# Optimization experiments

Measured on AMD Instinct MI355X. Metric: run time of the kernel, lower is better.

Reference implementation:

```python
import jax, jax.numpy as jnp
import numpy as np

B, IN, H = 16384, 1024, 1024


def setup_inputs() -> dict:
    key = jax.random.key(0)
    ks = jax.random.split(key, 7)
    s_in = 1.0 / np.sqrt(IN)
    s_h = 1.0 / np.sqrt(H)
    return {
        "x": jax.random.normal(ks[0], (B, IN), jnp.float32),
        "h0": jax.random.normal(ks[1], (B, H), jnp.float32),
        "c0": jax.random.normal(ks[2], (B, H), jnp.float32),
        # gate order along leading dim: f, i, o, g
        "wi": jax.random.uniform(ks[3], (4, H, IN), jnp.float32, -s_in, s_in),
        "bi": jax.random.uniform(ks[4], (4, H), jnp.float32, -s_in, s_in),
        "wh": jax.random.uniform(ks[5], (4, H, H), jnp.float32, -s_h, s_h),
        "bh": jax.random.uniform(ks[6], (4, H), jnp.float32, -s_h, s_h),
    }


def reference(x, h0, c0, wi, bi, wh, bh):
    # pre-activations for all 4 gates in two fused GEMMs: [b, 4, h]
    z = (jnp.einsum("bi,ghi->bgh", x, wi) + bi
         + jnp.einsum("bj,ghj->bgh", h0, wh) + bh)
    f = jax.nn.sigmoid(z[:, 0])   # forget gate
    i = jax.nn.sigmoid(z[:, 1])   # input gate
    o = jax.nn.sigmoid(z[:, 2])   # output gate
    g = jnp.tanh(z[:, 3])         # candidates
    ct = f * c0 + i * g
    ht = o * jnp.tanh(ct)
    return ht, ct
```

## Files before the change

### kernel.cpp

```cpp
#include <hip/hip_runtime.h>
#include <hip/hip_bf16.h>
#include <stdint.h>

#define B_ROWS 16384
#define K_DIM  2048
#define H_DIM  1024
#define N_DIM  4096
#define KB     (K_DIM * 2)
#define NT     (K_DIM / 64)
#define BUF0   0u
#define BUF1   65536u

using f32x4  = __attribute__((ext_vector_type(4))) float;
using bf16x8 = __attribute__((ext_vector_type(8))) __bf16;

__device__ __forceinline__ unsigned short f2bf(float f) {
    union { float f; unsigned u; } v; v.f = f;
    unsigned r = v.u + 0x7fffu + ((v.u >> 16) & 1u);
    return (unsigned short)(r >> 16);
}

__device__ __forceinline__ void gload16(const void* g, const void* l) {
    __builtin_amdgcn_global_load_lds(
        (const __attribute__((address_space(1))) void*)g,
        (__attribute__((address_space(3))) void*)l,
        16, 0, 0);
}

__device__ __forceinline__ float rcp1p(float e) {
    return __builtin_amdgcn_rcpf(1.f + e);
}

__global__ void pack_a_kernel(const float* __restrict__ x, const float* __restrict__ h0,
                              unsigned short* __restrict__ A) {
    int tid = blockIdx.x * 256 + threadIdx.x;
    int64_t idx = (int64_t)tid * 4;
    int b = (int)(idx >> 11);
    int k = (int)(idx & 2047);
    const float* src = (k < 1024) ? (x + (int64_t)b * 1024 + k)
                                  : (h0 + (int64_t)b * 1024 + (k - 1024));
    float4 v = *(const float4*)src;
    ushort4 o;
    o.x = f2bf(v.x); o.y = f2bf(v.y); o.z = f2bf(v.z); o.w = f2bf(v.w);
    *(ushort4*)(A + idx) = o;
}

__global__ void pack_w_kernel(const float* __restrict__ wi, const float* __restrict__ wh,
                              const float* __restrict__ bi, const float* __restrict__ bh,
                              unsigned short* __restrict__ W, float* __restrict__ bias) {
    int tid = blockIdx.x * 256 + threadIdx.x;
    int64_t idx = (int64_t)tid * 4;
    int r = (int)(idx >> 11);
    int k = (int)(idx & 2047);
    int h = r >> 2, g = r & 3;
    const float* src = (k < 1024)
        ? (wi + (int64_t)g * 1048576 + (int64_t)h * 1024 + k)
        : (wh + (int64_t)g * 1048576 + (int64_t)h * 1024 + (k - 1024));
    float4 v = *(const float4*)src;
    ushort4 o;
    o.x = f2bf(v.x); o.y = f2bf(v.y); o.z = f2bf(v.z); o.w = f2bf(v.w);
    *(ushort4*)(W + idx) = o;
    if (k == 0) bias[r] = bi[g * 1024 + h] + bh[g * 1024 + h];
}


#define FENCE   asm volatile("" ::: "memory")
#define BARRIER do { FENCE; __builtin_amdgcn_s_barrier(); FENCE; } while (0)
#define VM2     asm volatile("s_waitcnt vmcnt(2)" ::: "memory")
#define LGKM4   asm volatile("s_waitcnt lgkmcnt(4)" ::: "memory")
#define LGKM8   asm volatile("s_waitcnt lgkmcnt(8)" ::: "memory")
#define SP1     __builtin_amdgcn_s_setprio(1)
#define SP0     __builtin_amdgcn_s_setprio(0)

__global__ __launch_bounds__(512, 2) void lstm_gemm_fused(
    const unsigned short* __restrict__ A, const unsigned short* __restrict__ W,
    const float* __restrict__ bias, const float* __restrict__ c0,
    float* __restrict__ ht, float* __restrict__ ct)
{
    __shared__ char sm[131072];

    const int tid = threadIdx.x;
    const int l   = tid & 63;
    const int w   = tid >> 6;
    const int wm  = w >> 2;
    const int wn  = w & 3;

    const int bid = blockIdx.x;
    const int nid = (bid & 7) * 128 + (bid >> 3);
    const int bm  = nid >> 4;
    const int bn  = nid & 15;

    f32x4 acc[8][4];
#pragma unroll
    for (int i = 0; i < 8; ++i)
#pragma unroll
        for (int j = 0; j < 4; ++j) acc[i][j] = (f32x4){0.f, 0.f, 0.f, 0.f};

    const int srow = w * 16 + (l >> 2);
    const int scb  = ((l & 3) << 4) ^ (l & 32);
    const char* Asrc = (const char*)A + (size_t)(bm * 256 + srow) * KB + scb;
    const char* Wsrc = (const char*)W + (size_t)(bn * 256 + srow) * KB + scb;
    const uint32_t wL = (uint32_t)w * 1024u;

#define STAGE_A(KK, BOFF) do { \
    gload16(Asrc + (KK) * 64,            sm + (BOFF) + (KK) * 16384u + wL); \
    gload16(Asrc + (KK) * 64 + 128 * KB, sm + (BOFF) + (KK) * 16384u + 8192u + wL); \
} while (0)
#define STAGE_B(KK, BOFF) do { \
    gload16(Wsrc + (KK) * 64,            sm + (BOFF) + 32768u + (KK) * 16384u + wL); \
    gload16(Wsrc + (KK) * 64 + 128 * KB, sm + (BOFF) + 32768u + (KK) * 16384u + 8192u + wL); \
} while (0)
#define BUMP do { Asrc += 128; Wsrc += 128; } while (0)

    const int rr = l & 15, kg = l >> 4;
    const uint32_t loff = (uint32_t)rr * 64u + (((uint32_t)kg * 16u) ^ (uint32_t)((rr & 8) << 2));
    const uint32_t Ard = (uint32_t)wm * 8192u + loff;
    const uint32_t Brd = 32768u + (uint32_t)wn * 4096u + loff;

    bf16x8 aL0[4], aH0[4], aL1[4], aH1[4], bb0[4], bb1[4];

#define RD_A4(BOFF, KK, MB, ARR) do { \
    _Pragma("unroll") \
    for (int i_ = 0; i_ < 4; ++i_) \
        ARR[i_] = *(const bf16x8*)(sm + (BOFF) + (KK) * 16384u + Ard + ((MB) + i_) * 1024u); \
} while (0)
#define RD_B4(BOFF, KK, BRR) do { \
    _Pragma("unroll") \
    for (int i_ = 0; i_ < 4; ++i_) \
        BRR[i_] = *(const bf16x8*)(sm + (BOFF) + (KK) * 16384u + Brd + i_ * 1024u); \
} while (0)

#define MFMA16H(ARR, MB, BRR) do { \
    _Pragma("unroll") \
    for (int mf_ = 0; mf_ < 4; ++mf_) \
        _Pragma("unroll") \
        for (int nf_ = 0; nf_ < 4; ++nf_) \
            acc[(MB) + mf_][nf_] = __builtin_amdgcn_mfma_f32_16x16x32_bf16( \
                ARR[mf_], BRR[nf_], acc[(MB) + mf_][nf_], 0, 0, 0); \
} while (0)

    STAGE_A(0, BUF0); STAGE_B(0, BUF0);
    STAGE_A(1, BUF0); STAGE_B(1, BUF0);
    BUMP;
    asm volatile("s_waitcnt vmcnt(4)" ::: "memory");
    BARRIER;
    RD_A4(BUF0, 0, 0, aL0); RD_B4(BUF0, 0, bb0);

#define DO_TILE(CUR, NXT) do { \
     \
    RD_A4(CUR, 0, 4, aH0); \
    STAGE_A(0, NXT); \
    VM2; BARRIER; LGKM4; SP1; MFMA16H(aL0, 0, bb0); SP0; \
     \
    RD_A4(CUR, 1, 0, aL1); RD_B4(CUR, 1, bb1); \
    STAGE_B(0, NXT); \
    BARRIER; LGKM8; SP1; MFMA16H(aH0, 4, bb0); SP0; \
     \
    RD_A4(CUR, 1, 4, aH1); \
    STAGE_A(1, NXT); \
    VM2; BARRIER; LGKM4; SP1; MFMA16H(aL1, 0, bb1); SP0; \
     \
    RD_A4(NXT, 0, 0, aL0); RD_B4(NXT, 0, bb0); \
    STAGE_B(1, NXT); \
    BUMP; \
    BARRIER; LGKM8; SP1; MFMA16H(aH1, 4, bb1); SP0; \
} while (0)

#pragma unroll 1
    for (int tt = 0; tt < NT; tt += 2) {
        DO_TILE(BUF0, BUF1);
        DO_TILE(BUF1, BUF0);
    }

    asm volatile("s_waitcnt vmcnt(0) lgkmcnt(0)" ::: "memory");
    BARRIER;

    float* ep = (float*)(void*)sm + w * 1088;
    const int hbase = bn * 64 + wn * 16;
    const int rbase = bm * 256 + wm * 128;

#pragma unroll
    for (int mf = 0; mf < 8; ++mf) {
#pragma unroll
        for (int nf = 0; nf < 4; ++nf)
#pragma unroll
            for (int r = 0; r < 4; ++r)
                ep[((l >> 4) * 4 + r) * 68 + nf * 16 + (l & 15)] = acc[mf][nf][r];

#pragma unroll
        for (int it = 0; it < 4; ++it) {
            const int row = (l >> 4) + it * 4;
            const int hs  = l & 15;
            f32x4 z = *(const f32x4*)(ep + row * 68 + hs * 4);
            const int hg = hbase + hs;
            const float4 bz = ((const float4*)bias)[hg];
            const int brow = rbase + mf * 16 + row;

            float zf = z.x + bz.x;
            float zi = z.y + bz.y;
            float zo = z.z + bz.z;
            float zg = z.w + bz.w;

            float fg = rcp1p(__expf(-zf));
            float ig = rcp1p(__expf(-zi));
            float og = rcp1p(__expf(-zo));
            float gg = 2.f * rcp1p(__expf(-2.f * zg)) - 1.f;

            int64_t oi = (int64_t)brow * H_DIM + hg;
            float c  = fg * c0[oi] + ig * gg;
            float hh = og * (2.f * rcp1p(__expf(-2.f * c)) - 1.f);
            ct[oi] = c;
            ht[oi] = hh;
        }
    }
}

extern "C" void kernel_launch(void* const* d_in, const int* in_sizes, int n_in,
                              void* d_out, int out_size, void* d_ws, size_t ws_size,
                              hipStream_t stream) {
    const float* x  = (const float*)d_in[0];
    const float* h0 = (const float*)d_in[1];
    const float* c0 = (const float*)d_in[2];
    const float* wi = (const float*)d_in[3];
    const float* bi = (const float*)d_in[4];
    const float* wh = (const float*)d_in[5];
    const float* bh = (const float*)d_in[6];

    float* ht = (float*)d_out;
    float* ct = ht + (int64_t)B_ROWS * H_DIM;

    char* ws = (char*)d_ws;
    unsigned short* A  = (unsigned short*)ws;
    unsigned short* Wp = (unsigned short*)(ws + (64u << 20));
    float*          bs = (float*)(ws + (80u << 20));

    pack_a_kernel<<<32768, 256, 0, stream>>>(x, h0, A);
    pack_w_kernel<<<8192, 256, 0, stream>>>(wi, wh, bi, bh, Wp, bs);

    lstm_gemm_fused<<<1024, 512, 0, stream>>>(A, Wp, bs, c0, ht, ct);
}
```

Before: 306.5 us.

## Stagger wave groups with phase-shifted MFMA/LDS-read schedules to ping-pong

Splits the 8 waves into two groups by wm. One group keeps the original prefetch-ahead schedule. The other runs a phase-shifted schedule that issues MFMAs first and then LDS reads, with full lgkmcnt waits and sched_barriers. The goal is to interleave one group's matrix math with the other group's LDS reads, ping-pong style, to reduce contention for LDS and MFMA. The barrier counts must match between the two groups, and the full waits could expose LDS latency in the shifted group.

```diff
diff --git a/kernel.cpp b/kernel.cpp
--- a/kernel.cpp
+++ b/kernel.cpp
@@ -67,8 +67,10 @@
 #define FENCE   asm volatile("" ::: "memory")
 #define BARRIER do { FENCE; __builtin_amdgcn_s_barrier(); FENCE; } while (0)
 #define VM2     asm volatile("s_waitcnt vmcnt(2)" ::: "memory")
+#define LGKM0   asm volatile("s_waitcnt lgkmcnt(0)" ::: "memory")
 #define LGKM4   asm volatile("s_waitcnt lgkmcnt(4)" ::: "memory")
 #define LGKM8   asm volatile("s_waitcnt lgkmcnt(8)" ::: "memory")
+#define SCHED0  __builtin_amdgcn_sched_barrier(0)
 #define SP1     __builtin_amdgcn_s_setprio(1)
 #define SP0     __builtin_amdgcn_s_setprio(0)
 
@@ -146,30 +148,50 @@
     BARRIER;
     RD_A4(BUF0, 0, 0, aL0); RD_B4(BUF0, 0, bb0);
 
-#define DO_TILE(CUR, NXT) do { \
-     \
+#define DO_TILE_E(CUR, NXT) do { \
     RD_A4(CUR, 0, 4, aH0); \
     STAGE_A(0, NXT); \
     VM2; BARRIER; LGKM4; SP1; MFMA16H(aL0, 0, bb0); SP0; \
-     \
     RD_A4(CUR, 1, 0, aL1); RD_B4(CUR, 1, bb1); \
     STAGE_B(0, NXT); \
     BARRIER; LGKM8; SP1; MFMA16H(aH0, 4, bb0); SP0; \
-     \
     RD_A4(CUR, 1, 4, aH1); \
     STAGE_A(1, NXT); \
     VM2; BARRIER; LGKM4; SP1; MFMA16H(aL1, 0, bb1); SP0; \
-     \
     RD_A4(NXT, 0, 0, aL0); RD_B4(NXT, 0, bb0); \
     STAGE_B(1, NXT); \
     BUMP; \
     BARRIER; LGKM8; SP1; MFMA16H(aH1, 4, bb1); SP0; \
 } while (0)
 
+#define DO_TILE_O(CUR, NXT) do { \
+    STAGE_A(0, NXT); \
+    VM2; BARRIER; LGKM0; SP1; MFMA16H(aL0, 0, bb0); SP0; SCHED0; \
+    RD_A4(CUR, 0, 4, aH0); \
+    STAGE_B(0, NXT); \
+    BARRIER; LGKM0; SP1; MFMA16H(aH0, 4, bb0); SP0; SCHED0; \
+    RD_A4(CUR, 1, 0, aL1); RD_B4(CUR, 1, bb1); \
+    STAGE_A(1, NXT); \
+    VM2; BARRIER; LGKM0; SP1; MFMA16H(aL1, 0, bb1); SP0; SCHED0; \
+    RD_A4(CUR, 1, 4, aH1); \
+    STAGE_B(1, NXT); \
+    BUMP; \
+    BARRIER; LGKM0; SP1; MFMA16H(aH1, 4, bb1); SP0; SCHED0; \
+    RD_A4(NXT, 0, 0, aL0); RD_B4(NXT, 0, bb0); \
+} while (0)
+
+    if (wm == 0) {
 #pragma unroll 1
-    for (int tt = 0; tt < NT; tt += 2) {
-        DO_TILE(BUF0, BUF1);
-        DO_TILE(BUF1, BUF0);
+        for (int tt = 0; tt < NT; tt += 2) {
+            DO_TILE_E(BUF0, BUF1);
+            DO_TILE_E(BUF1, BUF0);
+        }
+    } else {
+#pragma unroll 1
+        for (int tt = 0; tt < NT; tt += 2) {
+            DO_TILE_O(BUF0, BUF1);
+            DO_TILE_O(BUF1, BUF0);
+        }
     }
 
     asm volatile("s_waitcnt vmcnt(0) lgkmcnt(0)" ::: "memory");
```

After: 305.9 us. About the same (-0.2%).

## Restructure GEMM main loop into quarter-tile MFMA phases with deeper A prefetch

Applied to the files above, without the earlier changes.

Rewrites the double-buffered main loop of the fused GEMM. A is now staged one tile ahead, and each 64-wide K tile is split into four MFMA quadrant phases (4x2 fragments over both K halves), separated by barriers and lgkmcnt(0) waits. The barrier and waitcnt macros drop their compiler memory fences. The goal is better overlap of global-to-LDS copies, LDS reads and MFMA work with lower register pressure. In exchange it doubles the barrier count per tile, and removing the memory clobbers risks the compiler reordering LDS accesses.

```diff
diff --git a/kernel.cpp b/kernel.cpp
--- a/kernel.cpp
+++ b/kernel.cpp
@@ -64,11 +64,10 @@
 }
 
 
-#define FENCE   asm volatile("" ::: "memory")
-#define BARRIER do { FENCE; __builtin_amdgcn_s_barrier(); FENCE; } while (0)
-#define VM2     asm volatile("s_waitcnt vmcnt(2)" ::: "memory")
-#define LGKM4   asm volatile("s_waitcnt lgkmcnt(4)" ::: "memory")
-#define LGKM8   asm volatile("s_waitcnt lgkmcnt(8)" ::: "memory")
+#define BAR     __builtin_amdgcn_s_barrier()
+#define LGKM0   asm volatile("s_waitcnt lgkmcnt(0)")
+#define LGKM8   asm volatile("s_waitcnt lgkmcnt(8)")
+#define VM4M    asm volatile("s_waitcnt vmcnt(4)" ::: "memory")
 #define SP1     __builtin_amdgcn_s_setprio(1)
 #define SP0     __builtin_amdgcn_s_setprio(0)
 
@@ -102,78 +101,83 @@
     const char* Wsrc = (const char*)W + (size_t)(bn * 256 + srow) * KB + scb;
     const uint32_t wL = (uint32_t)w * 1024u;
 
-#define STAGE_A(KK, BOFF) do { \
-    gload16(Asrc + (KK) * 64,            sm + (BOFF) + (KK) * 16384u + wL); \
-    gload16(Asrc + (KK) * 64 + 128 * KB, sm + (BOFF) + (KK) * 16384u + 8192u + wL); \
-} while (0)
-#define STAGE_B(KK, BOFF) do { \
-    gload16(Wsrc + (KK) * 64,            sm + (BOFF) + 32768u + (KK) * 16384u + wL); \
-    gload16(Wsrc + (KK) * 64 + 128 * KB, sm + (BOFF) + 32768u + (KK) * 16384u + 8192u + wL); \
-} while (0)
-#define BUMP do { Asrc += 128; Wsrc += 128; } while (0)
+#define STAGE_A2(SOFF, KK, BOFF) do { \
+    gload16(Asrc + (SOFF) + (KK) * 64,            sm + (BOFF) + (KK) * 16384u + wL); \
+    gload16(Asrc + (SOFF) + (KK) * 64 + 128 * KB, sm + (BOFF) + (KK) * 16384u + 8192u + wL); \
+} while (0)
+#define STAGE_B2(SOFF, KK, BOFF) do { \
+    gload16(Wsrc + (SOFF) + (KK) * 64,            sm + (BOFF) + 32768u + (KK) * 16384u + wL); \
+    gload16(Wsrc + (SOFF) + (KK) * 64 + 128 * KB, sm + (BOFF) + 32768u + (KK) * 16384u + 8192u + wL); \
+} while (0)
 
     const int rr = l & 15, kg = l >> 4;
     const uint32_t loff = (uint32_t)rr * 64u + (((uint32_t)kg * 16u) ^ (uint32_t)((rr & 8) << 2));
     const uint32_t Ard = (uint32_t)wm * 8192u + loff;
     const uint32_t Brd = 32768u + (uint32_t)wn * 4096u + loff;
 
-    bf16x8 aL0[4], aH0[4], aL1[4], aH1[4], bb0[4], bb1[4];
+    bf16x8 aA0[4], aA1[4], bL0[2], bL1[2], bH0[2], bH1[2];
 
 #define RD_A4(BOFF, KK, MB, ARR) do { \
     _Pragma("unroll") \
     for (int i_ = 0; i_ < 4; ++i_) \
         ARR[i_] = *(const bf16x8*)(sm + (BOFF) + (KK) * 16384u + Ard + ((MB) + i_) * 1024u); \
 } while (0)
-#define RD_B4(BOFF, KK, BRR) do { \
-    _Pragma("unroll") \
-    for (int i_ = 0; i_ < 4; ++i_) \
-        BRR[i_] = *(const bf16x8*)(sm + (BOFF) + (KK) * 16384u + Brd + i_ * 1024u); \
-} while (0)
-
-#define MFMA16H(ARR, MB, BRR) do { \
+#define RD_B2(BOFF, KK, NB, BRR) do { \
+    _Pragma("unroll") \
+    for (int i_ = 0; i_ < 2; ++i_) \
+        BRR[i_] = *(const bf16x8*)(sm + (BOFF) + (KK) * 16384u + Brd + ((NB) + i_) * 1024u); \
+} while (0)
+
+#define MMQ(MB, NB, BRR0, BRR1) do { \
     _Pragma("unroll") \
     for (int mf_ = 0; mf_ < 4; ++mf_) \
         _Pragma("unroll") \
-        for (int nf_ = 0; nf_ < 4; ++nf_) \
-            acc[(MB) + mf_][nf_] = __builtin_amdgcn_mfma_f32_16x16x32_bf16( \
-                ARR[mf_], BRR[nf_], acc[(MB) + mf_][nf_], 0, 0, 0); \
-} while (0)
-
-    STAGE_A(0, BUF0); STAGE_B(0, BUF0);
-    STAGE_A(1, BUF0); STAGE_B(1, BUF0);
-    BUMP;
-    asm volatile("s_waitcnt vmcnt(4)" ::: "memory");
-    BARRIER;
-    RD_A4(BUF0, 0, 0, aL0); RD_B4(BUF0, 0, bb0);
-
-#define DO_TILE(CUR, NXT) do { \
-     \
-    RD_A4(CUR, 0, 4, aH0); \
-    STAGE_A(0, NXT); \
-    VM2; BARRIER; LGKM4; SP1; MFMA16H(aL0, 0, bb0); SP0; \
-     \
-    RD_A4(CUR, 1, 0, aL1); RD_B4(CUR, 1, bb1); \
-    STAGE_B(0, NXT); \
-    BARRIER; LGKM8; SP1; MFMA16H(aH0, 4, bb0); SP0; \
-     \
-    RD_A4(CUR, 1, 4, aH1); \
-    STAGE_A(1, NXT); \
-    VM2; BARRIER; LGKM4; SP1; MFMA16H(aL1, 0, bb1); SP0; \
-     \
-    RD_A4(NXT, 0, 0, aL0); RD_B4(NXT, 0, bb0); \
-    STAGE_B(1, NXT); \
-    BUMP; \
-    BARRIER; LGKM8; SP1; MFMA16H(aH1, 4, bb1); SP0; \
-} while (0)
+        for (int nf_ = 0; nf_ < 2; ++nf_) \
+            acc[(MB) + mf_][(NB) + nf_] = __builtin_amdgcn_mfma_f32_16x16x32_bf16( \
+                aA0[mf_], BRR0[nf_], acc[(MB) + mf_][(NB) + nf_], 0, 0, 0); \
+    _Pragma("unroll") \
+    for (int mf_ = 0; mf_ < 4; ++mf_) \
+        _Pragma("unroll") \
+        for (int nf_ = 0; nf_ < 2; ++nf_) \
+            acc[(MB) + mf_][(NB) + nf_] = __builtin_amdgcn_mfma_f32_16x16x32_bf16( \
+                aA1[mf_], BRR1[nf_], acc[(MB) + mf_][(NB) + nf_], 0, 0, 0); \
+} while (0)
+
+    STAGE_A2(0, 0, BUF0); STAGE_A2(0, 1, BUF0);
+    STAGE_B2(0, 0, BUF0); STAGE_B2(0, 1, BUF0);
+    STAGE_A2(128, 0, BUF1); STAGE_A2(128, 1, BUF1);
+    VM4M;
+    BAR;
 
 #pragma unroll 1
-    for (int tt = 0; tt < NT; tt += 2) {
-        DO_TILE(BUF0, BUF1);
-        DO_TILE(BUF1, BUF0);
+    for (int it = 0; it < NT / 2; ++it) {
+        RD_A4(BUF0, 0, 0, aA0); RD_A4(BUF0, 1, 0, aA1);
+        RD_B2(BUF0, 0, 0, bL0); RD_B2(BUF0, 1, 0, bL1);
+        STAGE_B2(128, 0, BUF1); STAGE_B2(128, 1, BUF1);
+        LGKM8; BAR; LGKM0; SP1; MMQ(0, 0, bL0, bL1); SP0; BAR;
+        RD_B2(BUF0, 0, 2, bH0); RD_B2(BUF0, 1, 2, bH1);
+        BAR; LGKM0; SP1; MMQ(0, 2, bH0, bH1); SP0; BAR;
+        RD_A4(BUF0, 0, 4, aA0); RD_A4(BUF0, 1, 4, aA1);
+        BAR; LGKM0; SP1; MMQ(4, 2, bH0, bH1); SP0; BAR;
+        STAGE_A2(256, 0, BUF0); STAGE_A2(256, 1, BUF0);
+        BAR; LGKM0; SP1; MMQ(4, 0, bL0, bL1); SP0; VM4M; BAR;
+
+        RD_A4(BUF1, 0, 0, aA0); RD_A4(BUF1, 1, 0, aA1);
+        RD_B2(BUF1, 0, 0, bL0); RD_B2(BUF1, 1, 0, bL1);
+        STAGE_B2(256, 0, BUF0); STAGE_B2(256, 1, BUF0);
+        LGKM8; BAR; LGKM0; SP1; MMQ(0, 0, bL0, bL1); SP0; BAR;
+        RD_B2(BUF1, 0, 2, bH0); RD_B2(BUF1, 1, 2, bH1);
+        BAR; LGKM0; SP1; MMQ(0, 2, bH0, bH1); SP0; BAR;
+        RD_A4(BUF1, 0, 4, aA0); RD_A4(BUF1, 1, 4, aA1);
+        BAR; LGKM0; SP1; MMQ(4, 2, bH0, bH1); SP0; BAR;
+        STAGE_A2(384, 0, BUF1); STAGE_A2(384, 1, BUF1);
+        BAR; LGKM0; SP1; MMQ(4, 0, bL0, bL1); SP0; VM4M; BAR;
+
+        Asrc += 256; Wsrc += 256;
     }
 
     asm volatile("s_waitcnt vmcnt(0) lgkmcnt(0)" ::: "memory");
-    BARRIER;
+    BAR;
 
     float* ep = (float*)(void*)sm + w * 1088;
     const int hbase = bn * 64 + wn * 16;
@@ -188,8 +192,8 @@
                 ep[((l >> 4) * 4 + r) * 68 + nf * 16 + (l & 15)] = acc[mf][nf][r];
 
 #pragma unroll
-        for (int it = 0; it < 4; ++it) {
-            const int row = (l >> 4) + it * 4;
+        for (int itr = 0; itr < 4; ++itr) {
+            const int row = (l >> 4) + itr * 4;
             const int hs  = l & 15;
             f32x4 z = *(const f32x4*)(ep + row * 68 + hs * 4);
             const int hg = hbase + hs;
```

After: 310.5 us. Within noise of the previous version (+1.3%).
